# Performance work log

Measured on AMD Instinct MI355X. Metric: run time of the kernel, lower is better.

Reference implementation:

```python
import jax, jax.numpy as jnp
import numpy as np
from jax import lax

L, B, F = 1024, 2, 1024
E = 2
H = E * F          # ssm_features = 2048
N = 16             # state_dim
R = F // N         # dt_rank = 64
K = 4              # conv kernel size
DT_MIN, DT_MAX = 0.001, 0.1


def setup_inputs() -> dict:
    key = jax.random.key(0)
    ks = jax.random.split(key, 6)
    def w(k, shape, fan_in):
        return jax.random.normal(k, shape, jnp.float32) / np.float32(np.sqrt(fan_in))
    x = jax.random.normal(ks[0], (L, B, F), jnp.float32)
    W_in = w(ks[1], (F, 2 * H), F)
    W_conv = w(ks[2], (K, H // E, H), K * (H // E))  # flax Conv kernel (K, in/groups, out), groups=E
    b_conv = jnp.zeros((H,), jnp.float32)
    A_log = jnp.log(jnp.broadcast_to(jnp.arange(1, N + 1, dtype=jnp.float32), (H, N)))
    D = jnp.ones((H,), jnp.float32)
    W_ssm = w(ks[3], (H, R + 2 * N), H)
    W_dt = w(ks[4], (R, H), R)
    b_dt = jnp.zeros((H,), jnp.float32)
    W_out = w(ks[5], (H, F), H)
    return dict(x=x, W_in=W_in, W_conv=W_conv, b_conv=b_conv, A_log=A_log, D=D,
                W_ssm=W_ssm, W_dt=W_dt, b_dt=b_dt, W_out=W_out)


def _selective_scan(u, dt, A, Bm, Cm, D):
    # u, dt: (L,B,H); A: (H,N); Bm, Cm: (L,B,N); D: (H,)
    dt = jnp.clip(dt, DT_MIN, DT_MAX)
    dA = jnp.exp(jnp.einsum('lbh,hn->lbhn', dt, A))          # (L,B,H,N)
    dBu = jnp.einsum('lbh,lbn->lbhn', dt * u, Bm)            # (L,B,H,N)
    def comb(s, c):
        return (c[0] * s[0], c[0] * s[1] + c[1])
    _, xs = lax.associative_scan(comb, (dA, dBu), axis=0)
    y = jnp.einsum('lbn,lbhn->lbh', Cm, xs)
    return y + u * D


def reference(x, W_in, W_conv, b_conv, A_log, D, W_ssm, W_dt, b_dt, W_out):
    # in_proj (no bias) then split into ssm branch and gate residual
    h = x @ W_in                                             # (L,B,2H)
    xs, res = jnp.split(h, 2, axis=-1)                       # each (L,B,H)
    # causal grouped conv over time: rearrange (L,B,H)->(B,L,H), NWC layout
    xc = jnp.transpose(xs, (1, 0, 2))
    xc = lax.conv_general_dilated(
        xc, W_conv, window_strides=(1,), padding=[(K - 1, 0)],
        dimension_numbers=('NWC', 'WIO', 'NWC'), feature_group_count=E) + b_conv
    xs = jnp.transpose(xc, (1, 0, 2))                        # (L,B,H)
    u = jax.nn.silu(xs)
    # SSM
    A = -jnp.exp(A_log)                                      # (H,N)
    proj = u @ W_ssm                                         # (L,B,N+N+R)
    Bm = proj[..., :N]
    Cm = proj[..., N:2 * N]
    dt = proj[..., 2 * N:]
    delta = jax.nn.softplus(dt @ W_dt + b_dt)                # (L,B,H)
    y = _selective_scan(u, delta, A, Bm, Cm, D)
    # gate and out_proj (no bias)
    return (y * jax.nn.silu(res)) @ W_out                    # (L,B,F)
```

## Files before the change

kernel.cpp:

```cpp
#include <hip/hip_runtime.h>
#include <math.h>


typedef unsigned short u16;
typedef unsigned int u32;
typedef __attribute__((ext_vector_type(8))) short short8;
typedef __attribute__((ext_vector_type(4))) float floatx4;
typedef __attribute__((ext_vector_type(4))) u16 ushort4v;

__device__ __forceinline__ u16 f2bf(float f) {
    u32 u = __float_as_uint(f);
    return (u16)((u + 0x7fffu + ((u >> 16) & 1u)) >> 16);
}
__device__ __forceinline__ float bf2f(u16 v) {
    return __uint_as_float((u32)v << 16);
}
__device__ __forceinline__ float fexp2(float x) {
    return __builtin_amdgcn_exp2f(x);
}

__device__ __forceinline__ float dpp_red16(float v) {
    v += __uint_as_float((u32)__builtin_amdgcn_update_dpp(
        0, (int)__float_as_uint(v), 0xB1, 0xF, 0xF, true));
    v += __uint_as_float((u32)__builtin_amdgcn_update_dpp(
        0, (int)__float_as_uint(v), 0x4E, 0xF, 0xF, true));
    v += __uint_as_float((u32)__builtin_amdgcn_update_dpp(
        0, (int)__float_as_uint(v), 0x141, 0xF, 0xF, true));
    v += __uint_as_float((u32)__builtin_amdgcn_update_dpp(
        0, (int)__float_as_uint(v), 0x128, 0xF, 0xF, true));
    return v;
}

__device__ __forceinline__ void gl_lds16(const u16* g, u16* l) {
    auto gp = reinterpret_cast<const __attribute__((address_space(1))) u32*>(
        reinterpret_cast<uintptr_t>(g));
    auto lp = reinterpret_cast<__attribute__((address_space(3))) u32*>(
        reinterpret_cast<uintptr_t>(l));
    __builtin_amdgcn_global_load_lds(gp, lp, 16, 0, 0);
}

__device__ __forceinline__ void trans_dev(const float* __restrict__ S,
                                          u16* __restrict__ D, int R, int C,
                                          int bx, int by)
{
    __shared__ u16 t[64][65];
    int br = bx * 64;
    int bc = by * 64;
    int c = threadIdx.x & 63;
    int r0 = threadIdx.x >> 6;
#pragma unroll
    for (int i = 0; i < 16; ++i) {
        int r = r0 + i * 4;
        float v = 0.f;
        if (br + r < R && bc + c < C) v = S[(size_t)(br + r) * C + bc + c];
        t[r][c] = f2bf(v);
    }
    __syncthreads();
    int cc0 = threadIdx.x >> 4;
    int rr0 = (threadIdx.x & 15) * 4;
#pragma unroll
    for (int i = 0; i < 4; ++i) {
        int cc = i * 16 + cc0;
        if (bc + cc < C) {
            ushort4v o;
#pragma unroll
            for (int k = 0; k < 4; ++k) o[k] = t[rr0 + k][cc];
            *(ushort4v*)(D + (size_t)(bc + cc) * R + br + rr0) = o;
        }
    }
}

__global__ __launch_bounds__(256) void prep_k(
    const float* __restrict__ Wc, u16* __restrict__ WTc,
    const float* __restrict__ Wi, u16* __restrict__ WTi,
    const float* __restrict__ Wo, u16* __restrict__ WTo,
    const float* __restrict__ Ws, u16* __restrict__ WTs,
    const float* __restrict__ Wd, u16* __restrict__ WTd,
    const float* __restrict__ x,  u16* __restrict__ xb,
    float* __restrict__ outz)
{
    int b = blockIdx.x;
    if (b < 2048) { trans_dev(Wc, WTc, 4096, 2048, b & 63, b >> 6); return; }
    b -= 2048;
    if (b < 1024) { trans_dev(Wi, WTi, 1024, 4096, b & 15, b >> 4); return; }
    b -= 1024;
    if (b < 512)  { trans_dev(Wo, WTo, 2048, 1024, b & 31, b >> 5); return; }
    b -= 512;
    if (b < 64)   { trans_dev(Ws, WTs, 2048, 96,   b & 31, b >> 5); return; }
    b -= 64;
    if (b < 32)   { trans_dev(Wd, WTd, 64, 2048,   0,      b);      return; }
    b -= 32;
    if (b < 2048) {
        int i = (b * 256 + threadIdx.x) * 4;
        float4 v = *(const float4*)(x + i);
        u16 o[4] = {f2bf(v.x), f2bf(v.y), f2bf(v.z), f2bf(v.w)};
        *(ulong1*)(xb + i) = *(ulong1*)o;
        return;
    }
    b -= 2048;
    {
        int i = (b * 256 + threadIdx.x) * 4;
        *(float4*)(outz + i) = make_float4(0.f, 0.f, 0.f, 0.f);
    }
}

__global__ __launch_bounds__(256) void tbf_k(const u16* __restrict__ S,
                                             u16* __restrict__ D)
{
    __shared__ u16 t[64][68];
    int br = blockIdx.x * 64;
    int bc = blockIdx.y * 64;
    int c = threadIdx.x & 63;
    int r0 = threadIdx.x >> 6;
#pragma unroll
    for (int i = 0; i < 16; ++i) {
        int r = r0 + i * 4;
        t[r][c] = S[(size_t)(br + r) * 2048 + bc + c];
    }
    __syncthreads();
#pragma unroll
    for (int i = 0; i < 16; ++i) {
        int r = r0 + i * 4;
        D[(size_t)(bc + r) * 2048 + br + c] = t[c][r];
    }
}

template<int MODE>
__global__ __launch_bounds__(256) void gls_k(
    const u16* __restrict__ A, int lda,
    const u16* __restrict__ B, int ldb,
    float* __restrict__ Cf, int ldc,
    u16* __restrict__ Cb0, u16* __restrict__ Cb1, int nkt)
{
    __shared__ u16 As[128 * 64];
    __shared__ u16 Bs[64 * 64];
    const int tid = threadIdx.x;
    const int bm = blockIdx.y * 128;
    const int bn = blockIdx.x * 64;
    const int kofs = (MODE == 3) ? blockIdx.z * nkt * 64 : 0;
    const int lane = tid & 63, wave = tid >> 6, wm = wave * 32;
    const int m16 = lane & 15, q = lane >> 4;
    floatx4 acc[2][4] = {};

    const int rsub = lane >> 3;
    const int pch  = lane & 7;

    for (int kt = 0; kt < nkt; ++kt) {
        const int k0 = kofs + kt * 64;
#pragma unroll
        for (int i = 0; i < 4; ++i) {
            int r = i * 32 + wave * 8 + rsub;
            int c = pch ^ (r & 7);
            gl_lds16(A + (size_t)(bm + r) * lda + k0 + c * 8,
                     As + i * 2048 + wave * 512);
        }
#pragma unroll
        for (int i = 0; i < 2; ++i) {
            int r = i * 32 + wave * 8 + rsub;
            int c = pch ^ (r & 7);
            gl_lds16(B + (size_t)(bn + r) * ldb + k0 + c * 8,
                     Bs + i * 2048 + wave * 512);
        }
        __syncthreads();

#pragma unroll
        for (int ks = 0; ks < 2; ++ks) {
            short8 af[2], bfr[4];
#pragma unroll
            for (int ti = 0; ti < 2; ++ti) {
                int r = wm + ti * 16 + m16;
                int p = (ks * 4 + q) ^ (r & 7);
                af[ti] = *(const short8*)(As + r * 64 + p * 8);
            }
#pragma unroll
            for (int tj = 0; tj < 4; ++tj) {
                int r = tj * 16 + m16;
                int p = (ks * 4 + q) ^ (r & 7);
                bfr[tj] = *(const short8*)(Bs + r * 64 + p * 8);
            }
#pragma unroll
            for (int ti = 0; ti < 2; ++ti)
#pragma unroll
                for (int tj = 0; tj < 4; ++tj)
                    acc[ti][tj] = __builtin_amdgcn_mfma_f32_16x16x32_bf16(
                        af[ti], bfr[tj], acc[ti][tj], 0, 0, 0);
        }
        __syncthreads();
    }

    if (MODE == 3) {
#pragma unroll
        for (int tj = 0; tj < 4; ++tj) {
            int gn = bn + tj * 16 + m16;
#pragma unroll
            for (int ti = 0; ti < 2; ++ti) {
                int gm0 = bm + wm + ti * 16 + q * 4;
#pragma unroll
                for (int r = 0; r < 4; ++r)
                    atomicAdd(Cf + (size_t)(gm0 + r) * ldc + gn, acc[ti][tj][r]);
            }
        }
        return;
    }
    if (MODE == 0 && bn >= 2048) {
#pragma unroll
        for (int tj = 0; tj < 4; ++tj) {
            int gn = bn + tj * 16 + m16;
#pragma unroll
            for (int ti = 0; ti < 2; ++ti) {
                int gm0 = bm + wm + ti * 16 + q * 4;
                ushort4v h;
#pragma unroll
                for (int r = 0; r < 4; ++r) h[r] = f2bf(acc[ti][tj][r]);
                *(ushort4v*)(Cb1 + (size_t)(gn - 2048) * 2048 + gm0) = h;
            }
        }
        return;
    }
#pragma unroll
    for (int tj = 0; tj < 4; ++tj) {
#pragma unroll
        for (int ti = 0; ti < 2; ++ti) {
            int lr0 = wm + ti * 16 + q * 4;
#pragma unroll
            for (int r = 0; r < 4; ++r)
                As[(lr0 + r) * 64 + tj * 16 + m16] = f2bf(acc[ti][tj][r]);
        }
    }
    __syncthreads();
    {
        int row = tid >> 1, half = tid & 1;
        u16* gdst = Cb0 + (size_t)(bm + row) * 2048 + bn + half * 32;
        const u16* lsrc = As + row * 64 + half * 32;
#pragma unroll
        for (int i = 0; i < 4; ++i)
            *(short8*)(gdst + i * 8) = *(const short8*)(lsrc + i * 8);
    }
}

__global__ __launch_bounds__(256) void conv2_k(
    const u16* __restrict__ A,
    const u16* __restrict__ B,
    const float* __restrict__ bias,
    u16* __restrict__ Cb0,
    u16* __restrict__ Cb1,
    float* __restrict__ projz)
{
    __shared__ u16 Astrip[136 * 64];
    __shared__ u16 Bs[4 * 64 * 64];
    const int tid = threadIdx.x;
    const int bm = blockIdx.y * 128;
    const int bn = blockIdx.x * 64;
    {
        int fb = blockIdx.y * gridDim.x + blockIdx.x;
        *(float2*)(projz + fb * 512 + tid * 2) = make_float2(0.f, 0.f);
    }
    const int gofs = (bn >= 1024) ? 1024 : 0;
    const int lane = tid & 63, wave = tid >> 6, wm = wave * 32;
    const int m16 = lane & 15, q = lane >> 4;
    floatx4 acc[2][4] = {};
    const int rsub = lane >> 3;
    const int pch  = lane & 7;

    for (int ch = 0; ch < 16; ++ch) {
        const int ck = ch * 64;
#pragma unroll
        for (int i = 0; i < 4; ++i) {
            int r = i * 32 + wave * 8 + rsub;
            int c = pch ^ (r & 7);
            int rg = bm + r - 6;
            if (rg < 0) rg = 0;
            gl_lds16(A + (size_t)rg * 2048 + gofs + ck + c * 8,
                     Astrip + i * 2048 + wave * 512);
        }
        if (wave == 0) {
            int r = 128 + rsub;
            int c = pch ^ (r & 7);
            int rg = bm + r - 6;
            if (rg > 2047) rg = 2047;
            gl_lds16(A + (size_t)rg * 2048 + gofs + ck + c * 8,
                     Astrip + 4 * 2048);
        }
#pragma unroll
        for (int t = 0; t < 4; ++t)
#pragma unroll
            for (int i = 0; i < 2; ++i) {
                int r = i * 32 + wave * 8 + rsub;
                int c = pch ^ (r & 7);
                gl_lds16(B + (size_t)(bn + r) * 4096 + t * 1024 + ck + c * 8,
                         Bs + t * 4096 + i * 2048 + wave * 512);
            }
        if (bm == 0) {
            asm volatile("s_waitcnt vmcnt(0)" ::: "memory");
            if (tid < 48)
                *(short8*)(Astrip + (tid >> 3) * 64 + (tid & 7) * 8) = short8{};
        }
        __syncthreads();

#pragma unroll
        for (int t = 0; t < 4; ++t) {
#pragma unroll
            for (int ks = 0; ks < 2; ++ks) {
                short8 af[2], bfr[4];
#pragma unroll
                for (int ti = 0; ti < 2; ++ti) {
                    int sr = wm + ti * 16 + m16 + 2 * t;
                    int p = (ks * 4 + q) ^ (sr & 7);
                    af[ti] = *(const short8*)(Astrip + sr * 64 + p * 8);
                }
#pragma unroll
                for (int tj = 0; tj < 4; ++tj) {
                    int br = tj * 16 + m16;
                    int p = (ks * 4 + q) ^ (br & 7);
                    bfr[tj] = *(const short8*)(Bs + t * 4096 + br * 64 + p * 8);
                }
#pragma unroll
                for (int ti = 0; ti < 2; ++ti)
#pragma unroll
                    for (int tj = 0; tj < 4; ++tj)
                        acc[ti][tj] = __builtin_amdgcn_mfma_f32_16x16x32_bf16(
                            af[ti], bfr[tj], acc[ti][tj], 0, 0, 0);
            }
        }
        __syncthreads();
    }

#pragma unroll
    for (int tj = 0; tj < 4; ++tj) {
        int gn = bn + tj * 16 + m16;
        float bv = bias[gn];
#pragma unroll
        for (int ti = 0; ti < 2; ++ti) {
            int lr0 = wm + ti * 16 + q * 4;
            ushort4v h;
#pragma unroll
            for (int r = 0; r < 4; ++r) {
                float v = acc[ti][tj][r] + bv;
                v = v / (1.f + __expf(-v));
                u16 hv = f2bf(v);
                h[r] = hv;
                Astrip[(lr0 + r) * 64 + tj * 16 + m16] = hv;
            }
            *(ushort4v*)(Cb1 + (size_t)gn * 2048 + bm + lr0) = h;
        }
    }
    __syncthreads();
    {
        int row = tid >> 1, half = tid & 1;
        u16* gdst = Cb0 + (size_t)(bm + row) * 2048 + bn + half * 32;
        const u16* lsrc = Astrip + row * 64 + half * 32;
#pragma unroll
        for (int i = 0; i < 4; ++i)
            *(short8*)(gdst + i * 8) = *(const short8*)(lsrc + i * 8);
    }
}

#define APAD 40
__global__ __launch_bounds__(256) void g3_k(
    const u16* __restrict__ A,
    const u16* __restrict__ Bw,
    float* __restrict__ proj)
{
    __shared__ u16 As[128 * APAD];
    __shared__ u16 Bs[64 * APAD];
    const int tid = threadIdx.x;
    const int bn = blockIdx.x * 64;
    const int bm = blockIdx.y * 128;
    const int kb = blockIdx.z * 256;
    const int lane = tid & 63, wave = tid >> 6, wm = wave * 32;
    const int m16 = lane & 15, q = lane >> 4;
    floatx4 acc[2][4] = {};
    const int ar = tid >> 2, ac = (tid & 3) * 8;

    for (int kt = 0; kt < 8; ++kt) {
        const int k0 = kb + kt * 32;
#pragma unroll
        for (int p = 0; p < 2; ++p) {
            int r = ar + p * 64;
            *(short8*)(As + r * APAD + ac) =
                *(const short8*)(A + (size_t)(bm + r) * 2048 + k0 + ac);
        }
        *(short8*)(Bs + ar * APAD + ac) =
            *(const short8*)(Bw + (size_t)(bn + ar) * 2048 + k0 + ac);
        __syncthreads();

        short8 af[2], bfr[4];
#pragma unroll
        for (int ti = 0; ti < 2; ++ti)
            af[ti] = *(const short8*)(As + (wm + ti * 16 + m16) * APAD + q * 8);
#pragma unroll
        for (int tj = 0; tj < 4; ++tj)
            bfr[tj] = *(const short8*)(Bs + (tj * 16 + m16) * APAD + q * 8);
#pragma unroll
        for (int ti = 0; ti < 2; ++ti)
#pragma unroll
            for (int tj = 0; tj < 4; ++tj)
                acc[ti][tj] = __builtin_amdgcn_mfma_f32_16x16x32_bf16(
                    af[ti], bfr[tj], acc[ti][tj], 0, 0, 0);
        __syncthreads();
    }

#pragma unroll
    for (int tj = 0; tj < 4; ++tj) {
        int gn = bn + tj * 16 + m16;
        if (gn >= 96) continue;
        int col = (gn < 16) ? (2 * gn) : (gn < 32 ? 2 * (gn - 16) + 1 : 32 + gn);
#pragma unroll
        for (int ti = 0; ti < 2; ++ti)
#pragma unroll
            for (int r = 0; r < 4; ++r) {
                int gm = bm + wm + ti * 16 + q * 4 + r;
                atomicAdd(proj + (size_t)gm * 128 + col, acc[ti][tj][r]);
            }
    }
}

__global__ __launch_bounds__(256) void g4_k(
    const float* __restrict__ proj,
    const u16* __restrict__ B,
    const float* __restrict__ bias,
    float* __restrict__ Cf,
    u16* __restrict__ bc)
{
    __shared__ u16 As[128 * APAD];
    __shared__ u16 Bs[64 * APAD];
    const int tid = threadIdx.x;
    const int bm = blockIdx.y * 128;
    const int bn = blockIdx.x * 64;
    {
        int fb = blockIdx.y * gridDim.x + blockIdx.x;
        if (fb < 64) {
            int g = fb * 256 + tid;
            int m = g >> 3, i = (g & 7) * 4;
            float4 v = *(const float4*)(proj + (size_t)m * 128 + i);
            u16 o[4] = {f2bf(v.x), f2bf(v.y), f2bf(v.z), f2bf(v.w)};
            *(ulong1*)(bc + (size_t)m * 32 + i) = *(ulong1*)o;
        }
    }
    const int lane = tid & 63, wave = tid >> 6, wm = wave * 32;
    const int m16 = lane & 15, q = lane >> 4;
    floatx4 acc[2][4] = {};
    const int ar = tid >> 2, ac = (tid & 3) * 8;

    for (int kt = 0; kt < 2; ++kt) {
        const int k0 = kt * 32;
#pragma unroll
        for (int p = 0; p < 2; ++p) {
            int r = ar + p * 64;
            const float* src = proj + (size_t)(bm + r) * 128 + 64 + k0 + ac;
            float4 v0 = *(const float4*)src;
            float4 v1 = *(const float4*)(src + 4);
            short8 v = {(short)f2bf(v0.x), (short)f2bf(v0.y), (short)f2bf(v0.z),
                        (short)f2bf(v0.w), (short)f2bf(v1.x), (short)f2bf(v1.y),
                        (short)f2bf(v1.z), (short)f2bf(v1.w)};
            *(short8*)(As + r * APAD + ac) = v;
        }
        *(short8*)(Bs + ar * APAD + ac) =
            *(const short8*)(B + (size_t)(bn + ar) * 64 + k0 + ac);
        __syncthreads();
        short8 af[2], bfr[4];
#pragma unroll
        for (int ti = 0; ti < 2; ++ti)
            af[ti] = *(const short8*)(As + (wm + ti * 16 + m16) * APAD + q * 8);
#pragma unroll
        for (int tj = 0; tj < 4; ++tj)
            bfr[tj] = *(const short8*)(Bs + (tj * 16 + m16) * APAD + q * 8);
#pragma unroll
        for (int ti = 0; ti < 2; ++ti)
#pragma unroll
            for (int tj = 0; tj < 4; ++tj)
                acc[ti][tj] = __builtin_amdgcn_mfma_f32_16x16x32_bf16(
                    af[ti], bfr[tj], acc[ti][tj], 0, 0, 0);
        __syncthreads();
    }
#pragma unroll
    for (int tj = 0; tj < 4; ++tj) {
        int gn = bn + tj * 16 + m16;
        float bv = bias[gn];
#pragma unroll
        for (int ti = 0; ti < 2; ++ti) {
            int gm0 = bm + wm + ti * 16 + q * 4;
            float t[4];
#pragma unroll
            for (int r = 0; r < 4; ++r) {
                float v = acc[ti][tj][r] + bv;
                v = (v > 15.f) ? v : log1pf(__expf(v));
                t[r] = fminf(fmaxf(v, 0.001f), 0.1f);
            }
            *(float4*)(Cf + (size_t)gn * 2048 + gm0) =
                make_float4(t[0], t[1], t[2], t[3]);
        }
    }
}

__global__ __launch_bounds__(512) void scan7_k(
    const float* __restrict__ deltaT,
    const u16* __restrict__ uT,
    const u16* __restrict__ bc16,
    const float* __restrict__ A_log,
    const float* __restrict__ Dvec,
    const u16* __restrict__ resT,
    u16* __restrict__ zT)
{
    __shared__ float lP[2][32][16], lS[2][32][16], lI[2][32][16];
    __shared__ float yrow[2048];
    const int h = blockIdx.x;
    const int tid = threadIdx.x;
    const int n = tid & 15;
    const int c = tid >> 4;
    const int l0 = c * 32;

    const float An2 = -__expf(A_log[h * 16 + n]) * 1.442695041f;
    const float* drow = deltaT + (size_t)h * 2048;
    const u16*   urow = uT     + (size_t)h * 2048;

    float s0 = 0.f, s1 = 0.f, T0 = 0.f, T1 = 0.f;
    for (int j = 0; j < 32; ++j) {
        int l = l0 + j;
        float2 dtv = *(const float2*)(drow + 2 * l);
        u32 uv = *(const u32*)(urow + 2 * l);
        float uu0 = __uint_as_float(uv << 16);
        float uu1 = __uint_as_float(uv & 0xffff0000u);
        u32 w0 = *(const u32*)(bc16 + (size_t)(2 * l) * 32 + 2 * n);
        u32 w1 = *(const u32*)(bc16 + (size_t)(2 * l + 1) * 32 + 2 * n);
        float e0 = fexp2(dtv.x * An2);
        float e1 = fexp2(dtv.y * An2);
        s0 = fmaf(e0, s0, dtv.x * uu0 * __uint_as_float(w0 << 16));
        s1 = fmaf(e1, s1, dtv.y * uu1 * __uint_as_float(w1 << 16));
        T0 += dtv.x;
        T1 += dtv.y;
    }
    lP[0][c][n] = fexp2(T0 * An2); lS[0][c][n] = s0;
    lP[1][c][n] = fexp2(T1 * An2); lS[1][c][n] = s1;
    __syncthreads();
    if (tid < 32) {
        int bb = tid >> 4, nn = tid & 15;
        float X = 0.f;
#pragma unroll
        for (int cc = 0; cc < 32; ++cc) {
            lI[bb][cc][nn] = X;
            X = fmaf(lP[bb][cc][nn], X, lS[bb][cc][nn]);
        }
    }
    __syncthreads();

    s0 = lI[0][c][n];
    s1 = lI[1][c][n];
    const float Dh = Dvec[h];
    for (int j = 0; j < 32; ++j) {
        int l = l0 + j;
        float2 dtv = *(const float2*)(drow + 2 * l);
        u32 uv = *(const u32*)(urow + 2 * l);
        float uu0 = __uint_as_float(uv << 16);
        float uu1 = __uint_as_float(uv & 0xffff0000u);
        u32 w0 = *(const u32*)(bc16 + (size_t)(2 * l) * 32 + 2 * n);
        u32 w1 = *(const u32*)(bc16 + (size_t)(2 * l + 1) * 32 + 2 * n);
        float e0 = fexp2(dtv.x * An2);
        float e1 = fexp2(dtv.y * An2);
        s0 = fmaf(e0, s0, dtv.x * uu0 * __uint_as_float(w0 << 16));
        s1 = fmaf(e1, s1, dtv.y * uu1 * __uint_as_float(w1 << 16));
        float v0 = dpp_red16(__uint_as_float(w0 & 0xffff0000u) * s0);
        float v1 = dpp_red16(__uint_as_float(w1 & 0xffff0000u) * s1);
        if (n == 0) {
            yrow[2 * l]     = v0 + uu0 * Dh;
            yrow[2 * l + 1] = v1 + uu1 * Dh;
        }
    }
    __syncthreads();
    {
        int t0 = tid * 4;
        ushort4v rv = *(const ushort4v*)(resT + (size_t)h * 2048 + t0);
        u16 o[4];
#pragma unroll
        for (int i = 0; i < 4; ++i) {
            float r = bf2f(rv[i]);
            float y = yrow[t0 + i];
            o[i] = f2bf(y * (r / (1.f + __expf(-r))));
        }
        *(ulong1*)(zT + (size_t)h * 2048 + t0) = *(ulong1*)o;
    }
}

extern "C" void kernel_launch(void* const* d_in, const int* in_sizes, int n_in,
                              void* d_out, int out_size, void* d_ws, size_t ws_size,
                              hipStream_t stream)
{
    const float* x      = (const float*)d_in[0];
    const float* W_in   = (const float*)d_in[1];
    const float* W_conv = (const float*)d_in[2];
    const float* b_conv = (const float*)d_in[3];
    const float* A_log  = (const float*)d_in[4];
    const float* Dv     = (const float*)d_in[5];
    const float* W_ssm  = (const float*)d_in[6];
    const float* W_dt   = (const float*)d_in[7];
    const float* b_dt   = (const float*)d_in[8];
    const float* W_out  = (const float*)d_in[9];
    float* out = (float*)d_out;

    char* wsc = (char*)d_ws;
    u16*   xb     = (u16*)wsc;
    float* projb  = (float*)wsc;
    u16*   bc16   = (u16*)(wsc + (3u << 20));
    u16*   WT_in  = (u16*)(wsc + (4u << 20));
    u16*   u_mh   = (u16*)(wsc + (4u << 20));
    u16*   z_mh   = (u16*)(wsc + (4u << 20));
    u16*   xsbf   = (u16*)(wsc + (12u << 20));
    u16*   zT     = xsbf;
    u16*   resT   = (u16*)(wsc + (20u << 20));
    u16*   WT_cv  = (u16*)(wsc + (28u << 20));
    float* deltaT = (float*)(wsc + (28u << 20));
    u16*   uT     = (u16*)(wsc + (44u << 20));
    u16*   WT_out = (u16*)(wsc + (52u << 20));
    u16*   WT_ssm = (u16*)(wsc + (56u << 20));
    u16*   WT_dt  = (u16*)(wsc + (56u << 20) + (512u << 10));

    dim3 blk(256);

    prep_k<<<dim3(7776), blk, 0, stream>>>(
        W_conv, WT_cv, W_in, WT_in, W_out, WT_out, W_ssm, WT_ssm, W_dt, WT_dt,
        x, xb, out);

    gls_k<0><<<dim3(64, 16), blk, 0, stream>>>(
        xb, 1024, WT_in, 1024, nullptr, 0, xsbf, resT, 16);

    conv2_k<<<dim3(32, 16), blk, 0, stream>>>(
        xsbf, WT_cv, b_conv, u_mh, uT, projb);

    g3_k<<<dim3(2, 16, 8), blk, 0, stream>>>(u_mh, WT_ssm, projb);

    g4_k<<<dim3(32, 16), blk, 0, stream>>>(projb, WT_dt, b_dt, deltaT, bc16);

    scan7_k<<<dim3(2048), dim3(512), 0, stream>>>(
        deltaT, uT, bc16, A_log, Dv, resT, zT);

    tbf_k<<<dim3(32, 32), blk, 0, stream>>>(zT, z_mh);

    gls_k<3><<<dim3(16, 16, 2), blk, 0, stream>>>(
        z_mh, 2048, WT_out, 2048, out, 1024, nullptr, nullptr, 16);
}
```

Before: 311.6 us.

## Restructure scan kernel into finer chunks with per-thread multi-state registers

The selective-scan kernel now splits time into 128 chunks of 8 steps, with each thread holding 8 state dimensions for one batch. The old design had 32 chunks of 32 steps and one state per thread. The cross-chunk carry becomes a two-level scan in LDS (padded rows, group reductions, then a 32-thread serial pass). The C-weighted reduction is now done mostly in registers, with a single DPP swap instead of a 16-lane DPP tree. This is meant to shorten the serial dependency chains and cut per-step shuffle work, at the cost of more LDS traffic, more barriers and higher register pressure under the launch-bounds hint.

```diff
diff --git a/kernel.cpp b/kernel.cpp
--- a/kernel.cpp
+++ b/kernel.cpp
@@ -17,18 +17,6 @@
 }
 __device__ __forceinline__ float fexp2(float x) {
     return __builtin_amdgcn_exp2f(x);
-}
-
-__device__ __forceinline__ float dpp_red16(float v) {
-    v += __uint_as_float((u32)__builtin_amdgcn_update_dpp(
-        0, (int)__float_as_uint(v), 0xB1, 0xF, 0xF, true));
-    v += __uint_as_float((u32)__builtin_amdgcn_update_dpp(
-        0, (int)__float_as_uint(v), 0x4E, 0xF, 0xF, true));
-    v += __uint_as_float((u32)__builtin_amdgcn_update_dpp(
-        0, (int)__float_as_uint(v), 0x141, 0xF, 0xF, true));
-    v += __uint_as_float((u32)__builtin_amdgcn_update_dpp(
-        0, (int)__float_as_uint(v), 0x128, 0xF, 0xF, true));
-    return v;
 }
 
 __device__ __forceinline__ void gl_lds16(const u16* g, u16* l) {
@@ -493,7 +481,10 @@
     }
 }
 
-__global__ __launch_bounds__(512) void scan7_k(
+#define NCH 128
+#define CLEN 8
+#define SROW 129
+__global__ __launch_bounds__(512, 6) void scan8_k(
     const float* __restrict__ deltaT,
     const u16* __restrict__ uT,
     const u16* __restrict__ bc16,
@@ -502,71 +493,133 @@
     const u16* __restrict__ resT,
     u16* __restrict__ zT)
 {
-    __shared__ float lP[2][32][16], lS[2][32][16], lI[2][32][16];
+    __shared__ float sP[32 * SROW];
+    __shared__ float sS[32 * SROW];
+    __shared__ float tP[512], tS[512], eX[512];
     __shared__ float yrow[2048];
+
     const int h = blockIdx.x;
     const int tid = threadIdx.x;
-    const int n = tid & 15;
-    const int c = tid >> 4;
-    const int l0 = c * 32;
-
-    const float An2 = -__expf(A_log[h * 16 + n]) * 1.442695041f;
+    const int c  = tid >> 2;
+    const int b  = (tid >> 1) & 1;
+    const int ns = tid & 1;
+    const int mb = c * 16 + b;
+
     const float* drow = deltaT + (size_t)h * 2048;
     const u16*   urow = uT     + (size_t)h * 2048;
-
-    float s0 = 0.f, s1 = 0.f, T0 = 0.f, T1 = 0.f;
-    for (int j = 0; j < 32; ++j) {
-        int l = l0 + j;
-        float2 dtv = *(const float2*)(drow + 2 * l);
-        u32 uv = *(const u32*)(urow + 2 * l);
-        float uu0 = __uint_as_float(uv << 16);
-        float uu1 = __uint_as_float(uv & 0xffff0000u);
-        u32 w0 = *(const u32*)(bc16 + (size_t)(2 * l) * 32 + 2 * n);
-        u32 w1 = *(const u32*)(bc16 + (size_t)(2 * l + 1) * 32 + 2 * n);
-        float e0 = fexp2(dtv.x * An2);
-        float e1 = fexp2(dtv.y * An2);
-        s0 = fmaf(e0, s0, dtv.x * uu0 * __uint_as_float(w0 << 16));
-        s1 = fmaf(e1, s1, dtv.y * uu1 * __uint_as_float(w1 << 16));
-        T0 += dtv.x;
-        T1 += dtv.y;
-    }
-    lP[0][c][n] = fexp2(T0 * An2); lS[0][c][n] = s0;
-    lP[1][c][n] = fexp2(T1 * An2); lS[1][c][n] = s1;
+    const u16*   bcc  = bc16 + ns * 16;
+
+    float An2[8];
+    {
+        const float4 a0 = *(const float4*)(A_log + h * 16 + ns * 8);
+        const float4 a1 = *(const float4*)(A_log + h * 16 + ns * 8 + 4);
+        An2[0] = -__expf(a0.x) * 1.442695041f;
+        An2[1] = -__expf(a0.y) * 1.442695041f;
+        An2[2] = -__expf(a0.z) * 1.442695041f;
+        An2[3] = -__expf(a0.w) * 1.442695041f;
+        An2[4] = -__expf(a1.x) * 1.442695041f;
+        An2[5] = -__expf(a1.y) * 1.442695041f;
+        An2[6] = -__expf(a1.z) * 1.442695041f;
+        An2[7] = -__expf(a1.w) * 1.442695041f;
+    }
+
+    float x[8] = {};
+    float T = 0.f;
+#pragma unroll
+    for (int j = 0; j < CLEN; ++j) {
+        const int m = mb + 2 * j;
+        float dt = drow[m];
+        float uu = bf2f(urow[m]);
+        float dtu = dt * uu;
+        uint4 wa = *(const uint4*)(bcc + (size_t)m * 32);
+        uint4 wb = *(const uint4*)(bcc + (size_t)m * 32 + 8);
+        u32 wd[8] = {wa.x, wa.y, wa.z, wa.w, wb.x, wb.y, wb.z, wb.w};
+#pragma unroll
+        for (int k = 0; k < 8; ++k) {
+            float Bv = __uint_as_float(wd[k] << 16);
+            float e  = fexp2(dt * An2[k]);
+            x[k] = fmaf(e, x[k], dtu * Bv);
+        }
+        T += dt;
+    }
+    {
+        const int sq0 = b * 16 + ns * 8;
+#pragma unroll
+        for (int k = 0; k < 8; ++k) {
+            sP[(sq0 + k) * SROW + c] = fexp2(T * An2[k]);
+            sS[(sq0 + k) * SROW + c] = x[k];
+        }
+    }
+    __syncthreads();
+
+    {
+        const int sq = tid >> 4, sg = tid & 15;
+        const float* pp = sP + sq * SROW + sg * 8;
+        const float* ss = sS + sq * SROW + sg * 8;
+        float aP = 1.f, aS = 0.f;
+#pragma unroll
+        for (int i = 0; i < 8; ++i) {
+            float P = pp[i], S = ss[i];
+            aS = fmaf(P, aS, S);
+            aP *= P;
+        }
+        tP[sq * 16 + sg] = aP;
+        tS[sq * 16 + sg] = aS;
+    }
     __syncthreads();
     if (tid < 32) {
-        int bb = tid >> 4, nn = tid & 15;
         float X = 0.f;
 #pragma unroll
-        for (int cc = 0; cc < 32; ++cc) {
-            lI[bb][cc][nn] = X;
-            X = fmaf(lP[bb][cc][nn], X, lS[bb][cc][nn]);
-        }
-    }
-    __syncthreads();
-
-    s0 = lI[0][c][n];
-    s1 = lI[1][c][n];
+        for (int g = 0; g < 16; ++g) {
+            eX[tid * 16 + g] = X;
+            X = fmaf(tP[tid * 16 + g], X, tS[tid * 16 + g]);
+        }
+    }
+    __syncthreads();
+    {
+        const int sq = tid >> 4, sg = tid & 15;
+        float X = eX[sq * 16 + sg];
+        const float* pp = sP + sq * SROW + sg * 8;
+        float* ss = sS + sq * SROW + sg * 8;
+#pragma unroll
+        for (int i = 0; i < 8; ++i) {
+            float P = pp[i], S = ss[i];
+            ss[i] = X;
+            X = fmaf(P, X, S);
+        }
+    }
+    __syncthreads();
+    {
+        const int sq0 = b * 16 + ns * 8;
+#pragma unroll
+        for (int k = 0; k < 8; ++k) x[k] = sS[(sq0 + k) * SROW + c];
+    }
+
     const float Dh = Dvec[h];
-    for (int j = 0; j < 32; ++j) {
-        int l = l0 + j;
-        float2 dtv = *(const float2*)(drow + 2 * l);
-        u32 uv = *(const u32*)(urow + 2 * l);
-        float uu0 = __uint_as_float(uv << 16);
-        float uu1 = __uint_as_float(uv & 0xffff0000u);
-        u32 w0 = *(const u32*)(bc16 + (size_t)(2 * l) * 32 + 2 * n);
-        u32 w1 = *(const u32*)(bc16 + (size_t)(2 * l + 1) * 32 + 2 * n);
-        float e0 = fexp2(dtv.x * An2);
-        float e1 = fexp2(dtv.y * An2);
-        s0 = fmaf(e0, s0, dtv.x * uu0 * __uint_as_float(w0 << 16));
-        s1 = fmaf(e1, s1, dtv.y * uu1 * __uint_as_float(w1 << 16));
-        float v0 = dpp_red16(__uint_as_float(w0 & 0xffff0000u) * s0);
-        float v1 = dpp_red16(__uint_as_float(w1 & 0xffff0000u) * s1);
-        if (n == 0) {
-            yrow[2 * l]     = v0 + uu0 * Dh;
-            yrow[2 * l + 1] = v1 + uu1 * Dh;
-        }
-    }
-    __syncthreads();
+#pragma unroll
+    for (int j = 0; j < CLEN; ++j) {
+        const int m = mb + 2 * j;
+        float dt = drow[m];
+        float uu = bf2f(urow[m]);
+        float dtu = dt * uu;
+        uint4 wa = *(const uint4*)(bcc + (size_t)m * 32);
+        uint4 wb = *(const uint4*)(bcc + (size_t)m * 32 + 8);
+        u32 wd[8] = {wa.x, wa.y, wa.z, wa.w, wb.x, wb.y, wb.z, wb.w};
+        float y = 0.f;
+#pragma unroll
+        for (int k = 0; k < 8; ++k) {
+            float Bv = __uint_as_float(wd[k] << 16);
+            float Cv = __uint_as_float(wd[k] & 0xffff0000u);
+            float e  = fexp2(dt * An2[k]);
+            x[k] = fmaf(e, x[k], dtu * Bv);
+            y = fmaf(Cv, x[k], y);
+        }
+        float yo = y + __uint_as_float((u32)__builtin_amdgcn_update_dpp(
+            0, (int)__float_as_uint(y), 0xB1, 0xF, 0xF, true));
+        if (ns == 0) yrow[m] = yo + uu * Dh;
+    }
+    __syncthreads();
+
     {
         int t0 = tid * 4;
         ushort4v rv = *(const ushort4v*)(resT + (size_t)h * 2048 + t0);
@@ -630,7 +683,7 @@
 
     g4_k<<<dim3(32, 16), blk, 0, stream>>>(projb, WT_dt, b_dt, deltaT, bc16);
 
-    scan7_k<<<dim3(2048), dim3(512), 0, stream>>>(
+    scan8_k<<<dim3(2048), dim3(512), 0, stream>>>(
         deltaT, uT, bc16, A_log, Dv, resT, zT);
 
     tbf_k<<<dim3(32, 32), blk, 0, stream>>>(zT, z_mh);
```

Measured after the change: 296.7 us. 4.8% less time.
